# Kernel optimization log

Hardware: AMD Instinct MI355X
Metric: run time of the kernel (lower is better)

The kernel has to match this reference:

```python
import jax, jax.numpy as jnp
import numpy as np
import math

B, T = 8, 16
CODE_NUM = 1024
CODE_SIZE = 48
GRAPH_SIZE = 32
HIDDEN = 150      # hidden_size == t_output_size
T_ATTN = 32       # t_attention_size
DP_ATTN = 32      # DotProductAttention size
OUT = 1024


def _lin(k, fan_in, fan_out):
    s = 1.0 / math.sqrt(fan_in)
    kw, kb = jax.random.split(k)
    W = jax.random.uniform(kw, (fan_in, fan_out), minval=-s, maxval=s, dtype=jnp.float32)
    b = jax.random.uniform(kb, (fan_out,), minval=-s, maxval=s, dtype=jnp.float32)
    return W, b


def setup_inputs():
    key = jax.random.key(0)
    ks = jax.random.split(key, 16)
    u = jax.random.uniform(ks[0], (B, T, CODE_NUM))
    m1 = (u < 0.03).astype(jnp.float32)                   # persistent codes
    m2 = ((u >= 0.03) & (u < 0.05)).astype(jnp.float32)   # emerging neighbor codes
    m3 = ((u >= 0.05) & (u < 0.06)).astype(jnp.float32)   # emerging unrelated codes
    divided = jnp.stack([m1, m2, m3], axis=-1)            # [B,T,N,3], disjoint
    code_x = jnp.clip(m1 + m2 + m3, 0.0, 1.0)             # current-visit codes
    neighbors = ((u >= 0.06) & (u < 0.12)).astype(jnp.float32)
    lens = jax.random.randint(ks[1], (B,), T // 2, T + 1)
    a = (jax.random.uniform(ks[2], (CODE_NUM, CODE_NUM)) < 0.01).astype(jnp.float32)
    adj = a / (a.sum(axis=1, keepdims=True) + 1e-6)
    c_emb = jax.random.normal(ks[3], (CODE_NUM, CODE_SIZE)) * 0.05
    n_emb = jax.random.normal(ks[4], (CODE_NUM, CODE_SIZE)) * 0.05
    u_emb = jax.random.normal(ks[5], (CODE_NUM, GRAPH_SIZE)) * 0.05
    Wg, bg = _lin(ks[6], CODE_SIZE, GRAPH_SIZE)           # GraphLayer dense
    Wi, bi = _lin(ks[7], GRAPH_SIZE, 3 * HIDDEN)          # GRUCell input (r|z|n)
    Wh, bh = _lin(ks[8], HIDDEN, 3 * HIDDEN)              # GRUCell hidden (r|z|n)
    Wq, bq = _lin(ks[9], GRAPH_SIZE, T_ATTN)
    Wk, bk = _lin(ks[10], GRAPH_SIZE, T_ATTN)
    Wv, bv = _lin(ks[11], GRAPH_SIZE, HIDDEN)
    Wd, bd = _lin(ks[12], HIDDEN, DP_ATTN)                # DotProductAttention dense
    context = jax.random.normal(ks[13], (DP_ATTN,)) * 0.1
    Wc, bc = _lin(ks[14], HIDDEN, OUT)                    # Classifier
    return dict(code_x=code_x, divided=divided, neighbors=neighbors, lens=lens,
                adj=adj, c_emb=c_emb, n_emb=n_emb, u_emb=u_emb, Wg=Wg, bg=bg,
                Wi=Wi, bi=bi, Wh=Wh, bh=bh, Wq=Wq, bq=bq, Wk=Wk, bk=bk,
                Wv=Wv, bv=bv, Wd=Wd, bd=bd, context=context, Wc=Wc, bc=bc)


def _forward(code_x, divided, neighbors, lens, adj, c_emb, n_emb, u_emb,
             Wg, bg, Wi, bi, Wh, bh, Wq, bq, Wk, bk, Wv, bv, Wd, bd, context, Wc, bc):
    Bb, Tt, N = code_x.shape
    H = Wh.shape[0]
    NEG = -1e30
    scale = 1.0 / math.sqrt(Wq.shape[1])

    def step(carry, xs):
        h_prev, no_prev = carry                 # [B,N,H], [B,N,G]
        c_t, d_t, n_t, t_idx = xs               # [B,N], [B,N,3], [B,N], scalar
        c = c_t[..., None]
        nb = n_t[..., None]
        # GraphLayer: masked embeddings + one-hop adjacency aggregation
        ce = c * c_emb                           # [B,N,C]
        ne = nb * n_emb
        adj_ce = jnp.einsum('mn,bnc->bmc', adj, ce)
        adj_ne = jnp.einsum('mn,bnc->bmc', adj, ne)
        co = jax.nn.leaky_relu((ce + c * adj_ce + c * adj_ne) @ Wg + bg)      # [B,N,G]
        no = jax.nn.leaky_relu((ne + nb * adj_ne + nb * adj_ce) @ Wg + bg)

        m1 = d_t[..., 0]; m2 = d_t[..., 1]; m3 = d_t[..., 2]
        # TransitionLayer part 1: GRUCell on persistent (m1) codes; h_new starts at 0
        gi = co @ Wi + bi
        gh = h_prev @ Wh + bh
        i_r, i_z, i_n = jnp.split(gi, 3, axis=-1)
        h_r, h_z, h_n = jnp.split(gh, 3, axis=-1)
        r = jax.nn.sigmoid(i_r + h_r)
        z = jax.nn.sigmoid(i_z + h_z)
        n_g = jnp.tanh(i_n + r * h_n)
        h_m1 = (1.0 - z) * n_g + z * h_prev
        h_new = jnp.where(m1[..., None] > 0, h_m1, 0.0)

        # TransitionLayer part 2: single-head attention over emerging (m2|m3) codes, t>0
        m23 = (m2 + m3) > 0
        qrows = jnp.where(m2[..., None] > 0, no_prev,
                          jnp.where(m3[..., None] > 0, u_emb, 0.0))           # [B,N,G]
        q = qrows @ Wq + bq
        k = co @ Wk + bk
        v = qrows @ Wv + bv
        s = jnp.einsum('bia,bja->bij', q, k) * scale
        s = jnp.where(m23[:, None, :], s, NEG)   # keys restricted to m2|m3 set
        h_m23 = jnp.tanh(jnp.einsum('bij,bjh->bih', jax.nn.softmax(s, axis=-1), v))
        use23 = t_idx > 0
        h_new = jnp.where(jnp.logical_and(use23, m23)[..., None], h_m23, h_new)

        # per-step output: max-pool over each active subset (0 if subset empty)
        om1 = jnp.max(jnp.where(m1[..., None] > 0, h_m1, NEG), axis=1)
        om1 = jnp.where(jnp.any(m1 > 0, axis=1)[:, None], om1, 0.0)
        om23 = jnp.max(jnp.where(m23[..., None], h_m23, NEG), axis=1)
        om23 = jnp.where(jnp.logical_and(use23, jnp.any(m23, axis=1))[:, None], om23, 0.0)
        return (h_new, no), om1 + om23

    h0 = jnp.zeros((Bb, N, H), code_x.dtype)
    no0 = jnp.zeros((Bb, N, Wg.shape[1]), code_x.dtype)
    xs = (jnp.moveaxis(code_x, 1, 0), jnp.moveaxis(divided, 1, 0),
          jnp.moveaxis(neighbors, 1, 0), jnp.arange(Tt))
    _, outs = jax.lax.scan(step, (h0, no0), xs)
    outs = jnp.moveaxis(outs, 0, 1)              # [B,T,H]

    # DotProductAttention over (ragged) visit axis
    vu = (outs @ Wd + bd) @ context              # [B,T]
    tmask = jnp.arange(Tt)[None, :] < lens[:, None]
    score = jax.nn.softmax(jnp.where(tmask, vu, NEG), axis=-1)
    pooled = jnp.einsum('bth,bt->bh', outs, score)
    # Classifier (dropout_rate=0 -> identity) with sigmoid activation
    return jax.nn.sigmoid(pooled @ Wc + bc)


def reference(code_x, divided, neighbors, lens, adj, c_emb, n_emb, u_emb,
              Wg, bg, Wi, bi, Wh, bh, Wq, bq, Wk, bk, Wv, bv, Wd, bd, context, Wc, bc):
    return _forward(code_x, divided, neighbors, lens, adj, c_emb, n_emb, u_emb,
                    Wg, bg, Wi, bi, Wh, bh, Wq, bq, Wk, bk, Wv, bv, Wd, bd,
                    context, Wc, bc)
```

## Files before the change

### kernel.cpp

```cpp
#include <hip/hip_runtime.h>
#include <hip/hip_bf16.h>

#define Bq   8
#define Tq   16
#define Nq   1024
#define Cq   48
#define Gq   32
#define Hq   150
#define H3q  450
#define TAq  32
#define OUTq 1024
#define BTq  128

#define NC_CAP 128
#define NM_CAP 64
#define NACT   (2 * NC_CAP)
#define MTILE  16

__device__ __forceinline__ float lrelu(float x){ return x > 0.f ? x : 0.01f * x; }
__device__ __forceinline__ float sigm(float x){ return 1.f / (1.f + expf(-x)); }

__device__ int   g_n1[BTq], g_n23[BTq], g_nchain[BTq], g_nchain2[BTq];
__device__ short g_list1[BTq][NM_CAP];
__device__ short g_list23[BTq][NM_CAP];
__device__ short g_mapc[BTq][Nq];
__device__ short g_mapn[BTq][Nq];
__device__ int   g_chain[BTq][NM_CAP];
__device__ int   g_chain2[BTq][NM_CAP];
__device__ unsigned char g_cls[BTq][NM_CAP];
__device__ float g_Pc[Nq][Gq];
__device__ float g_Pn[Nq][Gq];
__device__ float g_co[BTq][NC_CAP][Gq];
__device__ float g_no[BTq][NC_CAP][Gq];
__device__ float g_gi[BTq][NM_CAP][H3q];
__device__ float g_vv[BTq][NM_CAP][Hq];
__device__ float g_hm23[BTq][NM_CAP][Hq];
__device__ float g_om23[BTq][Hq];
__device__ float g_hm1[BTq][NM_CAP][Hq];
__device__ float g_om1p[BTq][Hq];
__device__ float g_om1c[BTq][Hq];
__device__ float g_outs_unused[1];

__global__ __launch_bounds__(256) void k_pre(const float* c_emb, const float* n_emb, const float* Wg){
    int idx   = blockIdx.x * 256 + threadIdx.x;
    int which = idx >> 15;
    int r     = (idx >> 5) & 1023;
    int g     = idx & 31;
    const float* emb = which ? n_emb : c_emb;
    float acc = 0.f;
    for (int c = 0; c < Cq; ++c)
        acc += emb[r * Cq + c] * Wg[c * Gq + g];
    if (which) g_Pn[r][g] = acc; else g_Pc[r][g] = acc;
}

__global__ __launch_bounds__(512) void k_co(const float* code_x, const float* neighbors,
                                            const float* adj, const float* bg){
    int bt = blockIdx.x >> 1, half = blockIdx.x & 1, tid = threadIdx.x;
    __shared__ short lc_s[NC_CAP], ln_s[NC_CAP];
    __shared__ short act_s[NACT];
    __shared__ int nc_s, nn_s;
    __shared__ float Pact_s[NACT][Gq];
    __shared__ float A_s[MTILE][NACT];
    __shared__ short mrow_s[MTILE];
    int wave = tid >> 6, lane = tid & 63;

    if (wave == 0){
        int base = 0;
        for (int start = 0; start < Nq; start += 64){
            int n = start + lane;
            int pred = code_x[bt * Nq + n] > 0.f;
            unsigned long long mm = __ballot(pred);
            int pos = base + (int)__popcll(mm & ((1ull << lane) - 1ull));
            if (pred && pos < NC_CAP) lc_s[pos] = (short)n;
            base += (int)__popcll(mm);
        }
        if (lane == 0) nc_s = min(base, NC_CAP);
    } else if (wave == 1){
        int base = 0;
        for (int start = 0; start < Nq; start += 64){
            int n = start + lane;
            int pred = neighbors[bt * Nq + n] > 0.f;
            unsigned long long mm = __ballot(pred);
            int pos = base + (int)__popcll(mm & ((1ull << lane) - 1ull));
            if (pred && pos < NC_CAP) ln_s[pos] = (short)n;
            base += (int)__popcll(mm);
        }
        if (lane == 0) nn_s = min(base, NC_CAP);
    } else {
        if (half == 0) for (int n = tid - 128; n < Nq; n += 384) g_mapc[bt][n] = -1;
        else           for (int n = tid - 128; n < Nq; n += 384) g_mapn[bt][n] = -1;
    }
    __syncthreads();
    int nc = nc_s, nn = nn_s, total = nc + nn;

    for (int i = tid; i < total; i += 512) act_s[i] = (i < nc) ? lc_s[i] : ln_s[i - nc];
    if (half == 0) for (int i = tid; i < nc; i += 512) g_mapc[bt][lc_s[i]] = (short)i;
    else           for (int i = tid; i < nn; i += 512) g_mapn[bt][ln_s[i]] = (short)i;
    __syncthreads();

    for (int idx = tid; idx < total * Gq; idx += 512){
        int i = idx >> 5, g = idx & 31;
        Pact_s[i][g] = (i < nc) ? g_Pc[act_s[i]][g] : g_Pn[act_s[i]][g];
    }
    __syncthreads();

    int g = tid & 31, grp = tid >> 5;
    float bgv = bg[g];
    for (int rbase = half; rbase < total; rbase += 2 * MTILE){
        if (tid < MTILE){
            int r = rbase + 2 * tid;
            mrow_s[tid] = (r < total) ? act_s[r] : 0;
        }
        __syncthreads();
        int ntile = min(MTILE, (total - rbase + 1) / 2);
        for (int idx = tid; idx < ntile * total; idx += 512){
            int ti = idx / total, j = idx % total;
            A_s[ti][j] = adj[(size_t)mrow_s[ti] * Nq + act_s[j]];
        }
        __syncthreads();
        if (grp < ntile){
            int r = rbase + 2 * grp;
            float agg = 0.f;
            #pragma unroll 4
            for (int j = 0; j < total; ++j) agg += A_s[grp][j] * Pact_s[j][g];
            float v = lrelu(Pact_s[r][g] + agg + bgv);
            if (r < nc) g_co[bt][r][g]      = v;
            else        g_no[bt][r - nc][g] = v;
        }
        __syncthreads();
    }
}

__global__ __launch_bounds__(512) void k_mid(const float* divided, const float* u_emb,
                                             const float* Wi, const float* bi,
                                             const float* Wk, const float* bk,
                                             const float* Wq_, const float* bq_,
                                             const float* Wv_, const float* bv_,
                                             const float* bg){
    int bt = blockIdx.x, tid = threadIdx.x;
    int t = bt % Tq, btp = bt - 1;
    __shared__ short l1_s[NM_CAP], l23_s[NM_CAP];
    __shared__ int n1_s, n23_s;
    __shared__ float co1_s[NM_CAP][Gq];
    __shared__ float co23_s[NM_CAP][Gq];
    __shared__ float qr_s[NM_CAP][Gq];
    __shared__ float q_s[NM_CAP][TAq];
    __shared__ float k_s[NM_CAP][TAq];
    __shared__ float s_s[NM_CAP][NM_CAP];
    int wave = tid >> 6, lane = tid & 63;

    if (wave == 0){
        int base = 0;
        for (int start = 0; start < Nq; start += 64){
            int n = start + lane;
            int pred = divided[((size_t)bt * Nq + n) * 3 + 0] > 0.f;
            unsigned long long mm = __ballot(pred);
            int pos = base + (int)__popcll(mm & ((1ull << lane) - 1ull));
            if (pred && pos < NM_CAP) l1_s[pos] = (short)n;
            base += (int)__popcll(mm);
        }
        if (lane == 0) n1_s = min(base, NM_CAP);
    } else if (wave == 1){
        int base = 0;
        for (int start = 0; start < Nq; start += 64){
            int n = start + lane;
            float m2 = divided[((size_t)bt * Nq + n) * 3 + 1];
            float m3 = divided[((size_t)bt * Nq + n) * 3 + 2];
            int pred = (m2 > 0.f) || (m3 > 0.f);
            unsigned long long mm = __ballot(pred);
            int pos = base + (int)__popcll(mm & ((1ull << lane) - 1ull));
            if (pred && pos < NM_CAP) l23_s[pos] = (short)(n | (m2 > 0.f ? 0x400 : 0));
            base += (int)__popcll(mm);
        }
        if (lane == 0) n23_s = min(base, NM_CAP);
    }
    __syncthreads();
    int n1 = n1_s, n23 = n23_s;
    for (int i = tid; i < n1;  i += 512) g_list1[bt][i]  = l1_s[i];
    for (int i = tid; i < n23; i += 512) g_list23[bt][i] = l23_s[i];
    if (tid == 0){ g_n1[bt] = n1; g_n23[bt] = n23; }
    for (int idx = tid; idx < n1 * Gq; idx += 512){
        int i = idx >> 5, g = idx & 31;
        co1_s[i][g] = g_co[bt][g_mapc[bt][l1_s[i]]][g];
    }
    for (int idx = tid; idx < n23 * Gq; idx += 512){
        int i = idx >> 5, g = idx & 31;
        co23_s[i][g] = g_co[bt][g_mapc[bt][l23_s[i] & 1023]][g];
    }
    __syncthreads();

    if (tid < H3q){
        float wcol[Gq];
        #pragma unroll
        for (int g = 0; g < Gq; ++g) wcol[g] = Wi[g * H3q + tid];
        float bij = bi[tid];
        for (int i = 0; i < n1; ++i){
            float acc = bij;
            #pragma unroll
            for (int g = 0; g < Gq; ++g) acc += co1_s[i][g] * wcol[g];
            g_gi[bt][i][tid] = acc;
        }
    }
    if (t == 0 || n23 == 0) return;

    for (int idx = tid; idx < n23 * Gq; idx += 512){
        int i = idx >> 5, g = idx & 31;
        int e = l23_s[i], row = e & 1023;
        float qv;
        if (e & 0x400){
            int slot = g_mapn[btp][row];
            qv = (slot >= 0) ? g_no[btp][slot][g] : lrelu(bg[g]);
        } else {
            qv = u_emb[row * Gq + g];
        }
        qr_s[i][g] = qv;
    }
    __syncthreads();
    for (int idx = tid; idx < n23 * TAq; idx += 512){
        int i = idx >> 5, a = idx & 31;
        float acck = bk[a], accq = bq_[a];
        #pragma unroll
        for (int g = 0; g < Gq; ++g){
            acck += co23_s[i][g] * Wk[g * TAq + a];
            accq += qr_s[i][g] * Wq_[g * TAq + a];
        }
        k_s[i][a] = acck; q_s[i][a] = accq;
    }
    for (int idx = tid; idx < n23 * Hq; idx += 512){
        int i = idx / Hq, h = idx % Hq;
        float acc = bv_[h];
        #pragma unroll
        for (int g = 0; g < Gq; ++g) acc += qr_s[i][g] * Wv_[g * Hq + h];
        g_vv[bt][i][h] = acc;
    }
    __syncthreads();

    const float scale = 0.17677669529663687f;
    for (int idx = tid; idx < n23 * n23; idx += 512){
        int i = idx / n23, j = idx % n23;
        float acc = 0.f;
        #pragma unroll
        for (int a = 0; a < TAq; ++a) acc += q_s[i][a] * k_s[j][a];
        s_s[i][j] = acc * scale;
    }
    __syncthreads();
    for (int i = tid; i < n23; i += 512){
        float mx = -1e30f;
        for (int j = 0; j < n23; ++j) mx = fmaxf(mx, s_s[i][j]);
        float sum = 0.f;
        for (int j = 0; j < n23; ++j){ float e = expf(s_s[i][j] - mx); s_s[i][j] = e; sum += e; }
        float inv = 1.f / sum;
        for (int j = 0; j < n23; ++j) s_s[i][j] *= inv;
    }
    __syncthreads();
    for (int idx = tid; idx < n23 * Hq; idx += 512){
        int i = idx / Hq, h = idx % Hq;
        float acc = 0.f;
        for (int j = 0; j < n23; ++j) acc += s_s[i][j] * g_vv[bt][j][h];
        g_hm23[bt][i][h] = tanhf(acc);
    }
    __syncthreads();
    for (int h = tid; h < Hq; h += 512){
        float mx = -1e30f;
        for (int i = 0; i < n23; ++i) mx = fmaxf(mx, g_hm23[bt][i][h]);
        g_om23[bt][h] = mx;
    }
}

__global__ __launch_bounds__(512) void k_gru1(const float* Wh, const float* bh){
    int bt = blockIdx.x, tid = threadIdx.x;
    int t = bt % Tq, btp = bt - 1;
    __shared__ short map1p[Nq], map23p[Nq];
    __shared__ short l1_s[NM_CAP];
    __shared__ unsigned char cls_s[NM_CAP];
    __shared__ int m23l_s[NM_CAP];
    __shared__ int nf23_s;
    __shared__ float hb_s[Hq];
    __shared__ float ghf_s[H3q];
    __shared__ float hm1_s[NM_CAP][Hq];
    int n1 = g_n1[bt];
    for (int n = tid; n < Nq; n += 512){ map1p[n] = -1; map23p[n] = -1; }
    for (int i = tid; i < n1; i += 512) l1_s[i] = g_list1[bt][i];
    __syncthreads();
    if (t >= 1){
        int n1p = g_n1[btp];
        for (int i = tid; i < n1p; i += 512) map1p[g_list1[btp][i]] = (short)i;
        if (t >= 2){
            int n23p = g_n23[btp];
            for (int i = tid; i < n23p; i += 512) map23p[g_list23[btp][i] & 1023] = (short)i;
        }
    }
    __syncthreads();
    if (tid < 64){
        int i = tid;
        int cls = 0, sp = -1;
        if (i < n1 && t >= 1){
            int row = l1_s[i];
            if (map1p[row] >= 0){ cls = 1; sp = map1p[row]; }
            else if (t >= 2 && map23p[row] >= 0){ cls = 2; sp = map23p[row]; }
        }
        if (i < n1){ cls_s[i] = (unsigned char)cls; g_cls[bt][i] = (unsigned char)cls; }
        unsigned long long mch = __ballot(cls == 1);
        unsigned long long m23 = __ballot(cls == 2);
        int pch = (int)__popcll(mch & ((1ull << i) - 1ull));
        int p23 = (int)__popcll(m23 & ((1ull << i) - 1ull));
        if (cls == 1) g_chain[bt][pch] = (i << 16) | sp;
        if (cls == 2) m23l_s[p23] = (i << 16) | sp;
        if (i == 0){ nf23_s = (int)__popcll(m23); g_nchain[bt] = (int)__popcll(mch); }
    }
    __syncthreads();

    for (int idx = tid; idx < n1 * Hq; idx += 512){
        int i = idx / Hq, h = idx % Hq;
        if (cls_s[i] != 0) continue;
        float ir = g_gi[bt][i][h], iz = g_gi[bt][i][Hq + h], ig = g_gi[bt][i][2 * Hq + h];
        float r  = sigm(ir + bh[h]);
        float z  = sigm(iz + bh[Hq + h]);
        float ng = tanhf(ig + r * bh[2 * Hq + h]);
        hm1_s[i][h] = (1.f - z) * ng;
    }
    __syncthreads();

    int nf23 = nf23_s;
    for (int f = 0; f < nf23; ++f){
        int pk = m23l_s[f]; int i = pk >> 16, sp = pk & 0xffff;
        for (int h = tid; h < Hq; h += 512) hb_s[h] = g_hm23[btp][sp][h];
        __syncthreads();
        for (int j = tid; j < H3q; j += 512){
            float acc = bh[j];
            for (int k2 = 0; k2 < Hq; ++k2) acc += hb_s[k2] * Wh[k2 * H3q + j];
            ghf_s[j] = acc;
        }
        __syncthreads();
        for (int h = tid; h < Hq; h += 512){
            float ir = g_gi[bt][i][h], iz = g_gi[bt][i][Hq + h], ig = g_gi[bt][i][2 * Hq + h];
            float r  = sigm(ir + ghf_s[h]);
            float z  = sigm(iz + ghf_s[Hq + h]);
            float ng = tanhf(ig + r * ghf_s[2 * Hq + h]);
            hm1_s[i][h] = (1.f - z) * ng + z * hb_s[h];
        }
        __syncthreads();
    }

    for (int idx = tid; idx < n1 * Hq; idx += 512){
        int i = idx / Hq, h = idx % Hq;
        if (cls_s[i] != 1) g_hm1[bt][i][h] = hm1_s[i][h];
    }
    for (int h = tid; h < Hq; h += 512){
        float mx = -1e30f;
        for (int i = 0; i < n1; ++i) if (cls_s[i] != 1) mx = fmaxf(mx, hm1_s[i][h]);
        g_om1p[bt][h] = mx;
    }
}

__global__ __launch_bounds__(512) void k_gru1b(const float* Wh, const float* bh){
    int bt = blockIdx.x, tid = threadIdx.x;
    int t = bt % Tq, btp = bt - 1;
    __shared__ unsigned char defer_s[NM_CAP];
    __shared__ float hb_s[Hq];
    __shared__ float ghf_s[H3q];
    __shared__ float cmax_s[Hq];
    int nch = (t > 0) ? g_nchain[bt] : 0;
    for (int h = tid; h < Hq; h += 512) cmax_s[h] = -1e30f;
    if (tid < 64){
        int c = tid;
        int defer = 0;
        if (c < nch){
            int sp = g_chain[bt][c] & 0xffff;
            defer = (g_cls[btp][sp] == 1) ? 1 : 0;
            defer_s[c] = (unsigned char)defer;
        }
        unsigned long long md = __ballot((c < nch) && defer);
        int pos = (int)__popcll(md & ((1ull << c) - 1ull));
        if ((c < nch) && defer) g_chain2[bt][pos] = g_chain[bt][c];
        if (c == 0) g_nchain2[bt] = (int)__popcll(md);
    }
    __syncthreads();
    for (int c = 0; c < nch; ++c){
        if (defer_s[c]) continue;
        int pk = g_chain[bt][c]; int i = pk >> 16, sp = pk & 0xffff;
        for (int h = tid; h < Hq; h += 512) hb_s[h] = g_hm1[btp][sp][h];
        __syncthreads();
        for (int j = tid; j < H3q; j += 512){
            float acc = bh[j];
            for (int k2 = 0; k2 < Hq; ++k2) acc += hb_s[k2] * Wh[k2 * H3q + j];
            ghf_s[j] = acc;
        }
        __syncthreads();
        for (int h = tid; h < Hq; h += 512){
            float ir = g_gi[bt][i][h], iz = g_gi[bt][i][Hq + h], ig = g_gi[bt][i][2 * Hq + h];
            float r  = sigm(ir + ghf_s[h]);
            float z  = sigm(iz + ghf_s[Hq + h]);
            float ng = tanhf(ig + r * ghf_s[2 * Hq + h]);
            float v  = (1.f - z) * ng + z * hb_s[h];
            g_hm1[bt][i][h] = v;
            cmax_s[h] = fmaxf(cmax_s[h], v);
        }
        __syncthreads();
    }
    for (int h = tid; h < Hq; h += 512) g_om1c[bt][h] = cmax_s[h];
}

__global__ __launch_bounds__(512) void k_gru2(const float* Wh, const float* bh){
    int b = blockIdx.x, tid = threadIdx.x;
    __shared__ float hb_s[Hq];
    __shared__ float ghf_s[H3q];
    for (int t = 1; t < Tq; ++t){
        int bt = b * Tq + t, btp = bt - 1;
        int nch2 = g_nchain2[bt];
        for (int c = 0; c < nch2; ++c){
            int pk = g_chain2[bt][c]; int i = pk >> 16, sp = pk & 0xffff;
            for (int h = tid; h < Hq; h += 512) hb_s[h] = g_hm1[btp][sp][h];
            __syncthreads();
            for (int j = tid; j < H3q; j += 512){
                float acc = bh[j];
                for (int k2 = 0; k2 < Hq; ++k2) acc += hb_s[k2] * Wh[k2 * H3q + j];
                ghf_s[j] = acc;
            }
            __syncthreads();
            for (int h = tid; h < Hq; h += 512){
                float ir = g_gi[bt][i][h], iz = g_gi[bt][i][Hq + h], ig = g_gi[bt][i][2 * Hq + h];
                float r  = sigm(ir + ghf_s[h]);
                float z  = sigm(iz + ghf_s[Hq + h]);
                float ng = tanhf(ig + r * ghf_s[2 * Hq + h]);
                g_hm1[bt][i][h] = (1.f - z) * ng + z * hb_s[h];
            }
            __syncthreads();
        }
    }
}

__global__ __launch_bounds__(256) void k_final(const int* lens, const float* Wd, const float* bd,
                                               const float* ctx, const float* Wc, const float* bc,
                                               float* out){
    int b = blockIdx.x, tid = threadIdx.x;
    __shared__ float outs_s[Tq][Hq];
    __shared__ float wdc_s[Hq];
    __shared__ float score_s[Tq];
    __shared__ float pooled_s[Hq];
    for (int idx = tid; idx < Tq * Hq; idx += 256){
        int t = idx / Hq, h = idx % Hq;
        int bt = b * Tq + t;
        int n1 = g_n1[bt], n23 = (t > 0) ? g_n23[bt] : 0;
        float o = 0.f;
        if (n1 > 0){
            float mx = fmaxf(g_om1p[bt][h], g_om1c[bt][h]);
            int nd = (t > 0) ? g_nchain2[bt] : 0;
            for (int c = 0; c < nd; ++c){
                int i = g_chain2[bt][c] >> 16;
                mx = fmaxf(mx, g_hm1[bt][i][h]);
            }
            o = mx;
        }
        if (n23 > 0) o += g_om23[bt][h];
        outs_s[t][h] = o;
    }
    for (int h = tid; h < Hq; h += 256){
        float acc = 0.f;
        for (int d = 0; d < 32; ++d) acc += Wd[h * 32 + d] * ctx[d];
        wdc_s[h] = acc;
    }
    __syncthreads();
    int len = lens[b];
    if (tid < Tq){
        int t = tid;
        float acc = 0.f;
        for (int d = 0; d < 32; ++d) acc += bd[d] * ctx[d];
        for (int h = 0; h < Hq; ++h) acc += outs_s[t][h] * wdc_s[h];
        score_s[t] = (t < len) ? acc : -1e30f;
    }
    __syncthreads();
    if (tid == 0){
        float mx = -1e30f;
        for (int t = 0; t < Tq; ++t) mx = fmaxf(mx, score_s[t]);
        float sum = 0.f;
        for (int t = 0; t < Tq; ++t){ float e = expf(score_s[t] - mx); score_s[t] = e; sum += e; }
        float inv = 1.f / sum;
        for (int t = 0; t < Tq; ++t) score_s[t] *= inv;
    }
    __syncthreads();
    for (int h = tid; h < Hq; h += 256){
        float acc = 0.f;
        for (int t = 0; t < Tq; ++t) acc += score_s[t] * outs_s[t][h];
        pooled_s[h] = acc;
    }
    __syncthreads();
    for (int o = tid; o < OUTq; o += 256){
        float acc = bc[o];
        for (int h = 0; h < Hq; ++h) acc += pooled_s[h] * Wc[h * OUTq + o];
        out[b * OUTq + o] = sigm(acc);
    }
}

extern "C" void kernel_launch(void* const* d_in, const int* in_sizes, int n_in,
                              void* d_out, int out_size, void* d_ws, size_t ws_size,
                              hipStream_t stream){
    const float* code_x    = (const float*)d_in[0];
    const float* divided   = (const float*)d_in[1];
    const float* neighbors = (const float*)d_in[2];
    const int*   lens      = (const int*)  d_in[3];
    const float* adj       = (const float*)d_in[4];
    const float* c_emb     = (const float*)d_in[5];
    const float* n_emb     = (const float*)d_in[6];
    const float* u_emb     = (const float*)d_in[7];
    const float* Wg        = (const float*)d_in[8];
    const float* bg        = (const float*)d_in[9];
    const float* Wi        = (const float*)d_in[10];
    const float* bi        = (const float*)d_in[11];
    const float* Wh        = (const float*)d_in[12];
    const float* bh        = (const float*)d_in[13];
    const float* Wq_       = (const float*)d_in[14];
    const float* bq_       = (const float*)d_in[15];
    const float* Wk_       = (const float*)d_in[16];
    const float* bk_       = (const float*)d_in[17];
    const float* Wv_       = (const float*)d_in[18];
    const float* bv_       = (const float*)d_in[19];
    const float* Wd_       = (const float*)d_in[20];
    const float* bd_       = (const float*)d_in[21];
    const float* ctx       = (const float*)d_in[22];
    const float* Wc_       = (const float*)d_in[23];
    const float* bc_       = (const float*)d_in[24];
    float* out = (float*)d_out;

    hipLaunchKernelGGL(k_pre,   dim3(256),     dim3(256), 0, stream, c_emb, n_emb, Wg);
    hipLaunchKernelGGL(k_co,    dim3(2 * BTq), dim3(512), 0, stream, code_x, neighbors, adj, bg);
    hipLaunchKernelGGL(k_mid,   dim3(BTq),     dim3(512), 0, stream, divided, u_emb,
                       Wi, bi, Wk_, bk_, Wq_, bq_, Wv_, bv_, bg);
    hipLaunchKernelGGL(k_gru1,  dim3(BTq),     dim3(512), 0, stream, Wh, bh);
    hipLaunchKernelGGL(k_gru1b, dim3(BTq),     dim3(512), 0, stream, Wh, bh);
    hipLaunchKernelGGL(k_gru2,  dim3(Bq),      dim3(512), 0, stream, Wh, bh);
    hipLaunchKernelGGL(k_final, dim3(Bq),      dim3(256), 0, stream, lens, Wd_, bd_, ctx, Wc_, bc_, out);
}
```

Measured before the change: 287.1 us.

## Compute GRU input gates on the fly and fuse final pooling into gru2

Removes the precomputed g_gi buffer. Each GRU kernel now recomputes the input-gate projection (co row × Wi) where it is consumed, which drops a large global write and read in exchange for extra FLOPs inside the serial chain loops. The classifier/attention kernel is merged into the gru2 kernel, removing one launch, and padding is added to k_mid's shared arrays to avoid bank conflicts. The recomputation sits on the sequential critical path in k_gru2f and may lengthen it.

```diff
diff --git a/kernel.cpp b/kernel.cpp
--- a/kernel.cpp
+++ b/kernel.cpp
@@ -32,14 +32,25 @@
 __device__ float g_Pn[Nq][Gq];
 __device__ float g_co[BTq][NC_CAP][Gq];
 __device__ float g_no[BTq][NC_CAP][Gq];
-__device__ float g_gi[BTq][NM_CAP][H3q];
 __device__ float g_vv[BTq][NM_CAP][Hq];
 __device__ float g_hm23[BTq][NM_CAP][Hq];
 __device__ float g_om23[BTq][Hq];
 __device__ float g_hm1[BTq][NM_CAP][Hq];
 __device__ float g_om1p[BTq][Hq];
 __device__ float g_om1c[BTq][Hq];
-__device__ float g_outs_unused[1];
+
+__device__ __forceinline__ void gi3(const float* co_row, const float* Wi, const float* bi, int h,
+                                    float& gr, float& gz, float& gn){
+    gr = bi[h]; gz = bi[Hq + h]; gn = bi[2 * Hq + h];
+    #pragma unroll
+    for (int g = 0; g < Gq; ++g){
+        float c = co_row[g];
+        const float* w = Wi + g * H3q + h;
+        gr += c * w[0];
+        gz += c * w[Hq];
+        gn += c * w[2 * Hq];
+    }
+}
 
 __global__ __launch_bounds__(256) void k_pre(const float* c_emb, const float* n_emb, const float* Wg){
     int idx   = blockIdx.x * 256 + threadIdx.x;
@@ -132,7 +143,6 @@
 }
 
 __global__ __launch_bounds__(512) void k_mid(const float* divided, const float* u_emb,
-                                             const float* Wi, const float* bi,
                                              const float* Wk, const float* bk,
                                              const float* Wq_, const float* bq_,
                                              const float* Wv_, const float* bv_,
@@ -141,12 +151,11 @@
     int t = bt % Tq, btp = bt - 1;
     __shared__ short l1_s[NM_CAP], l23_s[NM_CAP];
     __shared__ int n1_s, n23_s;
-    __shared__ float co1_s[NM_CAP][Gq];
     __shared__ float co23_s[NM_CAP][Gq];
     __shared__ float qr_s[NM_CAP][Gq];
-    __shared__ float q_s[NM_CAP][TAq];
-    __shared__ float k_s[NM_CAP][TAq];
-    __shared__ float s_s[NM_CAP][NM_CAP];
+    __shared__ float q_s[NM_CAP][TAq + 1];
+    __shared__ float k_s[NM_CAP][TAq + 1];
+    __shared__ float s_s[NM_CAP][NM_CAP + 1];
     int wave = tid >> 6, lane = tid & 63;
 
     if (wave == 0){
@@ -179,30 +188,12 @@
     for (int i = tid; i < n1;  i += 512) g_list1[bt][i]  = l1_s[i];
     for (int i = tid; i < n23; i += 512) g_list23[bt][i] = l23_s[i];
     if (tid == 0){ g_n1[bt] = n1; g_n23[bt] = n23; }
-    for (int idx = tid; idx < n1 * Gq; idx += 512){
-        int i = idx >> 5, g = idx & 31;
-        co1_s[i][g] = g_co[bt][g_mapc[bt][l1_s[i]]][g];
-    }
+    if (t == 0 || n23 == 0) return;
+
     for (int idx = tid; idx < n23 * Gq; idx += 512){
         int i = idx >> 5, g = idx & 31;
         co23_s[i][g] = g_co[bt][g_mapc[bt][l23_s[i] & 1023]][g];
     }
-    __syncthreads();
-
-    if (tid < H3q){
-        float wcol[Gq];
-        #pragma unroll
-        for (int g = 0; g < Gq; ++g) wcol[g] = Wi[g * H3q + tid];
-        float bij = bi[tid];
-        for (int i = 0; i < n1; ++i){
-            float acc = bij;
-            #pragma unroll
-            for (int g = 0; g < Gq; ++g) acc += co1_s[i][g] * wcol[g];
-            g_gi[bt][i][tid] = acc;
-        }
-    }
-    if (t == 0 || n23 == 0) return;
-
     for (int idx = tid; idx < n23 * Gq; idx += 512){
         int i = idx >> 5, g = idx & 31;
         int e = l23_s[i], row = e & 1023;
@@ -267,7 +258,8 @@
     }
 }
 
-__global__ __launch_bounds__(512) void k_gru1(const float* Wh, const float* bh){
+__global__ __launch_bounds__(512) void k_gru1(const float* Wi, const float* bi,
+                                              const float* Wh, const float* bh){
     int bt = blockIdx.x, tid = threadIdx.x;
     int t = bt % Tq, btp = bt - 1;
     __shared__ short map1p[Nq], map23p[Nq];
@@ -275,6 +267,7 @@
     __shared__ unsigned char cls_s[NM_CAP];
     __shared__ int m23l_s[NM_CAP];
     __shared__ int nf23_s;
+    __shared__ float co1_s[NM_CAP][Gq];
     __shared__ float hb_s[Hq];
     __shared__ float ghf_s[H3q];
     __shared__ float hm1_s[NM_CAP][Hq];
@@ -308,15 +301,20 @@
         if (cls == 2) m23l_s[p23] = (i << 16) | sp;
         if (i == 0){ nf23_s = (int)__popcll(m23); g_nchain[bt] = (int)__popcll(mch); }
     }
+    for (int idx = tid; idx < n1 * Gq; idx += 512){
+        int i = idx >> 5, g = idx & 31;
+        co1_s[i][g] = g_co[bt][g_mapc[bt][l1_s[i]]][g];
+    }
     __syncthreads();
 
     for (int idx = tid; idx < n1 * Hq; idx += 512){
         int i = idx / Hq, h = idx % Hq;
         if (cls_s[i] != 0) continue;
-        float ir = g_gi[bt][i][h], iz = g_gi[bt][i][Hq + h], ig = g_gi[bt][i][2 * Hq + h];
-        float r  = sigm(ir + bh[h]);
-        float z  = sigm(iz + bh[Hq + h]);
-        float ng = tanhf(ig + r * bh[2 * Hq + h]);
+        float gr, gz, gn;
+        gi3(co1_s[i], Wi, bi, h, gr, gz, gn);
+        float r  = sigm(gr + bh[h]);
+        float z  = sigm(gz + bh[Hq + h]);
+        float ng = tanhf(gn + r * bh[2 * Hq + h]);
         hm1_s[i][h] = (1.f - z) * ng;
     }
     __syncthreads();
@@ -333,10 +331,11 @@
         }
         __syncthreads();
         for (int h = tid; h < Hq; h += 512){
-            float ir = g_gi[bt][i][h], iz = g_gi[bt][i][Hq + h], ig = g_gi[bt][i][2 * Hq + h];
-            float r  = sigm(ir + ghf_s[h]);
-            float z  = sigm(iz + ghf_s[Hq + h]);
-            float ng = tanhf(ig + r * ghf_s[2 * Hq + h]);
+            float gr, gz, gn;
+            gi3(co1_s[i], Wi, bi, h, gr, gz, gn);
+            float r  = sigm(gr + ghf_s[h]);
+            float z  = sigm(gz + ghf_s[Hq + h]);
+            float ng = tanhf(gn + r * ghf_s[2 * Hq + h]);
             hm1_s[i][h] = (1.f - z) * ng + z * hb_s[h];
         }
         __syncthreads();
@@ -353,10 +352,12 @@
     }
 }
 
-__global__ __launch_bounds__(512) void k_gru1b(const float* Wh, const float* bh){
+__global__ __launch_bounds__(512) void k_gru1b(const float* Wi, const float* bi,
+                                               const float* Wh, const float* bh){
     int bt = blockIdx.x, tid = threadIdx.x;
     int t = bt % Tq, btp = bt - 1;
     __shared__ unsigned char defer_s[NM_CAP];
+    __shared__ float co_s[Gq];
     __shared__ float hb_s[Hq];
     __shared__ float ghf_s[H3q];
     __shared__ float cmax_s[Hq];
@@ -379,6 +380,7 @@
     for (int c = 0; c < nch; ++c){
         if (defer_s[c]) continue;
         int pk = g_chain[bt][c]; int i = pk >> 16, sp = pk & 0xffff;
+        if (tid < Gq) co_s[tid] = g_co[bt][g_mapc[bt][g_list1[bt][i]]][tid];
         for (int h = tid; h < Hq; h += 512) hb_s[h] = g_hm1[btp][sp][h];
         __syncthreads();
         for (int j = tid; j < H3q; j += 512){
@@ -388,10 +390,11 @@
         }
         __syncthreads();
         for (int h = tid; h < Hq; h += 512){
-            float ir = g_gi[bt][i][h], iz = g_gi[bt][i][Hq + h], ig = g_gi[bt][i][2 * Hq + h];
-            float r  = sigm(ir + ghf_s[h]);
-            float z  = sigm(iz + ghf_s[Hq + h]);
-            float ng = tanhf(ig + r * ghf_s[2 * Hq + h]);
+            float gr, gz, gn;
+            gi3(co_s, Wi, bi, h, gr, gz, gn);
+            float r  = sigm(gr + ghf_s[h]);
+            float z  = sigm(gz + ghf_s[Hq + h]);
+            float ng = tanhf(gn + r * ghf_s[2 * Hq + h]);
             float v  = (1.f - z) * ng + z * hb_s[h];
             g_hm1[bt][i][h] = v;
             cmax_s[h] = fmaxf(cmax_s[h], v);
@@ -401,15 +404,25 @@
     for (int h = tid; h < Hq; h += 512) g_om1c[bt][h] = cmax_s[h];
 }
 
-__global__ __launch_bounds__(512) void k_gru2(const float* Wh, const float* bh){
+__global__ __launch_bounds__(512) void k_gru2f(const float* Wi, const float* bi,
+                                               const float* Wh, const float* bh,
+                                               const int* lens, const float* Wd, const float* bd,
+                                               const float* ctx, const float* Wc, const float* bc,
+                                               float* out){
     int b = blockIdx.x, tid = threadIdx.x;
+    __shared__ float co_s[Gq];
     __shared__ float hb_s[Hq];
     __shared__ float ghf_s[H3q];
+    __shared__ float outs_s[Tq][Hq];
+    __shared__ float wdc_s[Hq];
+    __shared__ float score_s[Tq];
+    __shared__ float pooled_s[Hq];
     for (int t = 1; t < Tq; ++t){
         int bt = b * Tq + t, btp = bt - 1;
         int nch2 = g_nchain2[bt];
         for (int c = 0; c < nch2; ++c){
             int pk = g_chain2[bt][c]; int i = pk >> 16, sp = pk & 0xffff;
+            if (tid < Gq) co_s[tid] = g_co[bt][g_mapc[bt][g_list1[bt][i]]][tid];
             for (int h = tid; h < Hq; h += 512) hb_s[h] = g_hm1[btp][sp][h];
             __syncthreads();
             for (int j = tid; j < H3q; j += 512){
@@ -419,26 +432,17 @@
             }
             __syncthreads();
             for (int h = tid; h < Hq; h += 512){
-                float ir = g_gi[bt][i][h], iz = g_gi[bt][i][Hq + h], ig = g_gi[bt][i][2 * Hq + h];
-                float r  = sigm(ir + ghf_s[h]);
-                float z  = sigm(iz + ghf_s[Hq + h]);
-                float ng = tanhf(ig + r * ghf_s[2 * Hq + h]);
+                float gr, gz, gn;
+                gi3(co_s, Wi, bi, h, gr, gz, gn);
+                float r  = sigm(gr + ghf_s[h]);
+                float z  = sigm(gz + ghf_s[Hq + h]);
+                float ng = tanhf(gn + r * ghf_s[2 * Hq + h]);
                 g_hm1[bt][i][h] = (1.f - z) * ng + z * hb_s[h];
             }
             __syncthreads();
         }
     }
-}
-
-__global__ __launch_bounds__(256) void k_final(const int* lens, const float* Wd, const float* bd,
-                                               const float* ctx, const float* Wc, const float* bc,
-                                               float* out){
-    int b = blockIdx.x, tid = threadIdx.x;
-    __shared__ float outs_s[Tq][Hq];
-    __shared__ float wdc_s[Hq];
-    __shared__ float score_s[Tq];
-    __shared__ float pooled_s[Hq];
-    for (int idx = tid; idx < Tq * Hq; idx += 256){
+    for (int idx = tid; idx < Tq * Hq; idx += 512){
         int t = idx / Hq, h = idx % Hq;
         int bt = b * Tq + t;
         int n1 = g_n1[bt], n23 = (t > 0) ? g_n23[bt] : 0;
@@ -455,7 +459,7 @@
         if (n23 > 0) o += g_om23[bt][h];
         outs_s[t][h] = o;
     }
-    for (int h = tid; h < Hq; h += 256){
+    for (int h = tid; h < Hq; h += 512){
         float acc = 0.f;
         for (int d = 0; d < 32; ++d) acc += Wd[h * 32 + d] * ctx[d];
         wdc_s[h] = acc;
@@ -479,13 +483,13 @@
         for (int t = 0; t < Tq; ++t) score_s[t] *= inv;
     }
     __syncthreads();
-    for (int h = tid; h < Hq; h += 256){
+    for (int h = tid; h < Hq; h += 512){
         float acc = 0.f;
         for (int t = 0; t < Tq; ++t) acc += score_s[t] * outs_s[t][h];
         pooled_s[h] = acc;
     }
     __syncthreads();
-    for (int o = tid; o < OUTq; o += 256){
+    for (int o = tid; o < OUTq; o += 512){
         float acc = bc[o];
         for (int h = 0; h < Hq; ++h) acc += pooled_s[h] * Wc[h * OUTq + o];
         out[b * OUTq + o] = sigm(acc);
@@ -525,9 +529,9 @@
     hipLaunchKernelGGL(k_pre,   dim3(256),     dim3(256), 0, stream, c_emb, n_emb, Wg);
     hipLaunchKernelGGL(k_co,    dim3(2 * BTq), dim3(512), 0, stream, code_x, neighbors, adj, bg);
     hipLaunchKernelGGL(k_mid,   dim3(BTq),     dim3(512), 0, stream, divided, u_emb,
-                       Wi, bi, Wk_, bk_, Wq_, bq_, Wv_, bv_, bg);
-    hipLaunchKernelGGL(k_gru1,  dim3(BTq),     dim3(512), 0, stream, Wh, bh);
-    hipLaunchKernelGGL(k_gru1b, dim3(BTq),     dim3(512), 0, stream, Wh, bh);
-    hipLaunchKernelGGL(k_gru2,  dim3(Bq),      dim3(512), 0, stream, Wh, bh);
-    hipLaunchKernelGGL(k_final, dim3(Bq),      dim3(256), 0, stream, lens, Wd_, bd_, ctx, Wc_, bc_, out);
-}
+                       Wk_, bk_, Wq_, bq_, Wv_, bv_, bg);
+    hipLaunchKernelGGL(k_gru1,  dim3(BTq),     dim3(512), 0, stream, Wi, bi, Wh, bh);
+    hipLaunchKernelGGL(k_gru1b, dim3(BTq),     dim3(512), 0, stream, Wi, bi, Wh, bh);
+    hipLaunchKernelGGL(k_gru2f, dim3(Bq),      dim3(512), 0, stream, Wi, bi, Wh, bh,
+                       lens, Wd_, bd_, ctx, Wc_, bc_, out);
+}
```

After: 298.0 us. +3.8%, slower.
